# Optimization experiments

Measured on AMD Instinct MI355X. Metric: run time of the kernel, lower is better.

The kernel has to match this reference:

```python
import jax, jax.numpy as jnp
import numpy as np

HIDDEN = 1024
N_HEAD = 16
D_HEAD = HIDDEN // N_HEAD


def setup_inputs() -> dict:
    key = jax.random.key(0)
    ks = jax.random.split(key, 12)
    B, S, H = 2, 2048, HIDDEN
    scale = 1.0 / np.sqrt(H)
    inp = {
        "q": jax.random.normal(ks[0], (B, S, H), jnp.float32),
        "k": jax.random.normal(ks[1], (B, S, H), jnp.float32),
        "v": jax.random.normal(ks[2], (B, S, H), jnp.float32),
        "mask": jnp.ones((B, 1, S, S), jnp.int32),
        "w_q": jax.random.normal(ks[3], (H, H), jnp.float32) * scale,
        "b_q": jnp.zeros((H,), jnp.float32),
        "w_k": jax.random.normal(ks[4], (H, H), jnp.float32) * scale,
        "b_k": jnp.zeros((H,), jnp.float32),
        "w_v": jax.random.normal(ks[5], (H, H), jnp.float32) * scale,
        "b_v": jnp.zeros((H,), jnp.float32),
        "w_o": jax.random.normal(ks[6], (H, H), jnp.float32) * scale,
        "b_o": jnp.zeros((H,), jnp.float32),
    }
    return inp


def reference(q, k, v, mask, w_q, b_q, w_k, b_k, w_v, b_v, w_o, b_o):
    B, Sq, H = q.shape
    Sk = k.shape[1]
    # projections (weights stored as [in, out])
    qh = (q @ w_q + b_q).reshape(B, Sq, N_HEAD, D_HEAD).transpose(0, 2, 1, 3)
    kh = (k @ w_k + b_k).reshape(B, Sk, N_HEAD, D_HEAD).transpose(0, 2, 1, 3)
    vh = (v @ w_v + b_v).reshape(B, Sk, N_HEAD, D_HEAD).transpose(0, 2, 1, 3)
    scores = jnp.einsum("bhqd,bhkd->bhqk", qh, kh) * (D_HEAD ** -0.5)
    scores = jnp.where(mask == 0, jnp.float32(-10000.0), scores)
    attn = jax.nn.softmax(scores, axis=-1)
    out = jnp.einsum("bhqk,bhkd->bhqd", attn, vh)
    out = out.transpose(0, 2, 1, 3).reshape(B, Sq, H)
    return out @ w_o + b_o
```

## Files before the change

kernel.cpp:

```cpp
#include <hip/hip_runtime.h>
#include <hip/hip_bf16.h>
#include <stdint.h>

#define S_LEN 2048
#define HID   1024
#define NHEAD 16
#define DHEAD 64
#define BATCH 2

#define QSCALE 0.18033688f
#define MASKNEG -14427.0f

typedef __bf16 bf16_t;
typedef __bf16 bf16x4 __attribute__((ext_vector_type(4)));
typedef __bf16 bf16x8 __attribute__((ext_vector_type(8)));
typedef float  f32x4  __attribute__((ext_vector_type(4)));


__device__ __forceinline__ void gl_lds16(const bf16_t* g, bf16_t* l) {
  __builtin_amdgcn_global_load_lds((const __attribute__((address_space(1))) void*)g,
                                   (__attribute__((address_space(3))) void*)l,
                                   16, 0, 0);
}

template<int TR, int TC, int NW = 4>
__device__ __forceinline__ void stage_tile(const bf16_t* __restrict__ g, int ldg,
                                           bf16_t* lds, int wave, int lane) {
  constexpr int CH = TC / 8;
  constexpr int NINST = (TR * CH) / 64;
  #pragma unroll
  for (int i = wave; i < NINST; i += NW) {
    int slot = i * 64 + lane;
    int r  = slot / CH;
    int cs = slot & (CH - 1);
    int c  = cs ^ (r & (CH - 1));
    gl_lds16(g + (size_t)r * ldg + c * 8, lds + i * 512);
  }
}

template<int CH>
__device__ __forceinline__ bf16x8 frag_ld(const bf16_t* lds, int row, int kchunk) {
  int cs = kchunk ^ (row & (CH - 1));
  return *(const bf16x8*)(lds + (row * CH + cs) * 8);
}

__global__ __launch_bounds__(256) void preamble(
    const float* __restrict__ q, const float* __restrict__ k, const float* __restrict__ v,
    bf16_t* __restrict__ qb, bf16_t* __restrict__ kb, bf16_t* __restrict__ vb,
    const float* __restrict__ w0, const float* __restrict__ w1,
    const float* __restrict__ w2, const float* __restrict__ w3,
    bf16_t* __restrict__ wt, const int* __restrict__ mask, int* __restrict__ flags) {
  __shared__ float t[64][65];
  __shared__ int oks[16];
  int id = blockIdx.x;
  if (id < 12288) {
    int which = id >> 12;
    const float* src = which == 0 ? q : which == 1 ? k : v;
    bf16_t* dst = which == 0 ? qb : which == 1 ? kb : vb;
    size_t i = (((size_t)(id & 4095)) * 256 + threadIdx.x) * 4;
    float4 u = *(const float4*)(src + i);
    bf16x4 o = {(bf16_t)u.x, (bf16_t)u.y, (bf16_t)u.z, (bf16_t)u.w};
    *(bf16x4*)(dst + i) = o;
  } else if (id < 13312) {
    int tt = id - 12288;
    int bx = tt & 15, by = (tt >> 4) & 15, bz = tt >> 8;
    const float* W = bz == 0 ? w0 : bz == 1 ? w1 : bz == 2 ? w2 : w3;
    bf16_t* WT = wt + (size_t)bz * HID * HID;
    int tx = threadIdx.x & 63, ty = threadIdx.x >> 6;
    int r0 = by * 64, c0 = bx * 64;
    #pragma unroll
    for (int i = ty; i < 64; i += 4) t[i][tx] = W[(size_t)(r0 + i) * HID + c0 + tx];
    __syncthreads();
    #pragma unroll
    for (int i = ty; i < 64; i += 4) WT[(size_t)(c0 + i) * HID + r0 + tx] = (bf16_t)t[tx][i];
  } else {
    int tt = id - 13312;
    int qtile = tt & 15, rg = (tt >> 4) & 7, b = tt >> 7;
    const int* base = mask + (size_t)b * S_LEN * S_LEN
                    + (size_t)(qtile * 128 + rg * 16) * S_LEN;
    int tid = threadIdx.x;
    int kt = tid >> 4;
    int ok = 1;
    #pragma unroll
    for (int r = 0; r < 16; ++r) {
      const int4* p = (const int4*)(base + (size_t)r * S_LEN + tid * 8);
      int4 a = p[0], c = p[1];
      ok &= (a.x != 0) & (a.y != 0) & (a.z != 0) & (a.w != 0) &
            (c.x != 0) & (c.y != 0) & (c.z != 0) & (c.w != 0);
    }
    if (tid < 16) oks[tid] = -1;
    __syncthreads();
    if (!ok) atomicAnd(&oks[kt], 0);
    __syncthreads();
    if (tid < 16 && oks[tid] == 0) atomicAnd(&flags[(b * 16 + qtile) * 16 + tid], 0);
  }
}

__global__ __launch_bounds__(512) void qkv_gemm(
    const bf16_t* __restrict__ qb, const bf16_t* __restrict__ kb, const bf16_t* __restrict__ vb,
    const bf16_t* __restrict__ wT,
    const float* __restrict__ bq, const float* __restrict__ bk, const float* __restrict__ bv,
    bf16_t* __restrict__ Qh, bf16_t* __restrict__ Kh, bf16_t* __restrict__ VhT) {
  int mode = blockIdx.z;
  const bf16_t* A    = mode == 0 ? qb : mode == 1 ? kb : vb;
  const bf16_t* Bt   = wT + (size_t)mode * HID * HID;
  const float*  bias = mode == 0 ? bq : mode == 1 ? bk : bv;

  __shared__ __align__(16) bf16_t As[128 * 64];
  __shared__ __align__(16) bf16_t Bs[128 * 64];

  int tid = threadIdx.x, wave = tid >> 6, lane = tid & 63;
  int lane15 = lane & 15, quad = lane >> 4;
  int m0 = blockIdx.x * 128, n0 = blockIdx.y * 128;
  int wm = (wave & 3) * 32, wn = (wave >> 2) * 64;

  f32x4 zero4 = {0.f, 0.f, 0.f, 0.f};
  f32x4 acc[2][4];
  #pragma unroll
  for (int t = 0; t < 2; ++t)
    #pragma unroll
    for (int n = 0; n < 4; ++n) acc[t][n] = zero4;

  for (int k0 = 0; k0 < HID; k0 += 64) {
    stage_tile<128, 64, 8>(A  + (size_t)m0 * HID + k0, HID, As, wave, lane);
    stage_tile<128, 64, 8>(Bt + (size_t)n0 * HID + k0, HID, Bs, wave, lane);
    __syncthreads();
    #pragma unroll
    for (int kc = 0; kc < 2; ++kc) {
      bf16x8 af[2], bfr[4];
      #pragma unroll
      for (int t = 0; t < 2; ++t) af[t]  = frag_ld<8>(As, wm + t * 16 + lane15, kc * 4 + quad);
      #pragma unroll
      for (int n = 0; n < 4; ++n) bfr[n] = frag_ld<8>(Bs, wn + n * 16 + lane15, kc * 4 + quad);
      if (mode < 2) {
        #pragma unroll
        for (int t = 0; t < 2; ++t)
          #pragma unroll
          for (int n = 0; n < 4; ++n)
            acc[t][n] = __builtin_amdgcn_mfma_f32_16x16x32_bf16(af[t], bfr[n], acc[t][n], 0, 0, 0);
      } else {
        #pragma unroll
        for (int t = 0; t < 2; ++t)
          #pragma unroll
          for (int n = 0; n < 4; ++n)
            acc[t][n] = __builtin_amdgcn_mfma_f32_16x16x32_bf16(bfr[n], af[t], acc[t][n], 0, 0, 0);
      }
    }
    __syncthreads();
  }

  if (mode < 2) {
    float sc = (mode == 0) ? QSCALE : 1.0f;
    bf16_t* dst = (mode == 0 ? Qh : Kh);
    #pragma unroll
    for (int t = 0; t < 2; ++t) {
      #pragma unroll
      for (int n = 0; n < 4; ++n) {
        int col = n0 + wn + n * 16 + lane15;
        float bb = bias[col];
        #pragma unroll
        for (int i = 0; i < 4; ++i) {
          int row = m0 + wm + t * 16 + quad * 4 + i;
          bf16_t o = (bf16_t)((acc[t][n][i] + bb) * sc);
          int b = row >> 11, s = row & 2047;
          int h = col >> 6,  d = col & 63;
          dst[((size_t)(b * NHEAD + h) * S_LEN + s) * DHEAD + d] = o;
        }
      }
    }
  } else {
    #pragma unroll
    for (int n = 0; n < 4; ++n) {
      int dbase = n0 + wn + n * 16 + quad * 4;
      float4 bb4 = *(const float4*)(bias + dbase);
      #pragma unroll
      for (int t = 0; t < 2; ++t) {
        int token = m0 + wm + t * 16 + lane15;
        int b = token >> 11, s = token & 2047;
        #pragma unroll
        for (int i = 0; i < 4; ++i) {
          int dg = dbase + i;
          int h = dg >> 6, d = dg & 63;
          float bb = i == 0 ? bb4.x : i == 1 ? bb4.y : i == 2 ? bb4.z : bb4.w;
          VhT[((size_t)(b * NHEAD + h) * DHEAD + d) * S_LEN + s] = (bf16_t)(acc[t][n][i] + bb);
        }
      }
    }
  }
}

__global__ __launch_bounds__(512) void attn_kernel(
    const bf16_t* __restrict__ Qh, const bf16_t* __restrict__ Kh, const bf16_t* __restrict__ VhT,
    const int* __restrict__ mask, const int* __restrict__ flags,
    bf16_t* __restrict__ O) {
  __shared__ __align__(16) bf16_t Ks[4][64 * 64];
  __shared__ __align__(16) bf16_t VTs[4][64 * 64];
  __shared__ __align__(16) bf16_t Ps[128 * 64];

  int tid = threadIdx.x, wave = tid >> 6, lane = tid & 63;
  int lane15 = lane & 15, quad = lane >> 4;
  int L = blockIdx.x + (blockIdx.y << 4);
  int xcd = L & 7, slot = L >> 3;
  int bh = xcd + ((slot >> 4) << 3);
  int qt = slot & 15;
  int b = bh >> 4, h = bh & 15;
  int wrow = wave << 4;

  const bf16_t* Kbase = Kh + (size_t)bh * S_LEN * DHEAD;
  const bf16_t* Vbase = VhT + (size_t)bh * DHEAD * S_LEN;
  const int* flagrow = flags + (b * 16 + qt) * 16;

  int fmask = 0;
  #pragma unroll
  for (int j = 0; j < 16; ++j) fmask |= (flagrow[j] == 0 ? 1 : 0) << j;

  stage_tile<128, 64, 8>(Qh + ((size_t)bh * S_LEN + qt * 128) * DHEAD, DHEAD, Ps, wave, lane);
  stage_tile<64, 64, 8>(Kbase, DHEAD, Ks[0], wave, lane);
  stage_tile<64, 64, 8>(Vbase, S_LEN, VTs[0], wave, lane);
  stage_tile<64, 64, 8>(Kbase + (size_t)64 * DHEAD, DHEAD, Ks[1], wave, lane);
  stage_tile<64, 64, 8>(Vbase + 64, S_LEN, VTs[1], wave, lane);
  asm volatile("s_waitcnt vmcnt(4)" ::: "memory");
  __builtin_amdgcn_s_barrier();

  bf16x8 qa[2];
  #pragma unroll
  for (int kc = 0; kc < 2; ++kc)
    qa[kc] = frag_ld<8>(Ps, wrow + lane15, kc * 4 + quad);

  bf16x8 ones8;
  #pragma unroll
  for (int j = 0; j < 8; ++j) ones8[j] = (bf16_t)1.0f;

  f32x4 zero4 = {0.f, 0.f, 0.f, 0.f};
  f32x4 o_acc[5];
  #pragma unroll
  for (int mt = 0; mt < 5; ++mt) o_acc[mt] = zero4;

  for (int kt = 0; kt < S_LEN / 64; ++kt) {
    int nt = kt + 2 <= 31 ? kt + 2 : 31;
    int nbuf = (kt + 2) & 3;
    stage_tile<64, 64, 8>(Kbase + (size_t)nt * 64 * DHEAD, DHEAD, Ks[nbuf], wave, lane);
    stage_tile<64, 64, 8>(Vbase + nt * 64, S_LEN, VTs[nbuf], wave, lane);
    asm volatile("s_waitcnt vmcnt(4)" ::: "memory");
    __builtin_amdgcn_s_barrier();

    const bf16_t* Kc = Ks[kt & 3];
    const bf16_t* Vc = VTs[kt & 3];

    f32x4 sa[4];
    {
      bf16x8 kf[4];
      #pragma unroll
      for (int mc = 0; mc < 4; ++mc) kf[mc] = frag_ld<8>(Kc, mc * 16 + lane15, quad);
      __builtin_amdgcn_s_setprio(1);
      #pragma unroll
      for (int mc = 0; mc < 4; ++mc)
        sa[mc] = __builtin_amdgcn_mfma_f32_16x16x32_bf16(kf[mc], qa[0], zero4, 0, 0, 0);
      __builtin_amdgcn_s_setprio(0);
      #pragma unroll
      for (int mc = 0; mc < 4; ++mc) kf[mc] = frag_ld<8>(Kc, mc * 16 + lane15, 4 + quad);
      __builtin_amdgcn_s_setprio(1);
      #pragma unroll
      for (int mc = 0; mc < 4; ++mc)
        sa[mc] = __builtin_amdgcn_mfma_f32_16x16x32_bf16(kf[mc], qa[1], sa[mc], 0, 0, 0);
      __builtin_amdgcn_s_setprio(0);
    }

    if ((fmask >> (kt >> 1)) & 1) {
      int q = qt * 128 + wrow + lane15;
      #pragma unroll
      for (int mc = 0; mc < 4; ++mc)
        #pragma unroll
        for (int i = 0; i < 4; ++i) {
          int c = kt * 64 + mc * 16 + quad * 4 + i;
          if (mask[(size_t)b * S_LEN * S_LEN + (size_t)q * S_LEN + c] == 0)
            sa[mc][i] = MASKNEG;
        }
    }

    {
      int q = wrow + lane15;
      #pragma unroll
      for (int mc = 0; mc < 4; ++mc) {
        bf16x4 pk = {(bf16_t)exp2f(sa[mc][0]), (bf16_t)exp2f(sa[mc][1]),
                     (bf16_t)exp2f(sa[mc][2]), (bf16_t)exp2f(sa[mc][3])};
        int chunk = mc * 2 + (quad >> 1);
        int slot = chunk ^ (q & 7);
        *(bf16x4*)(Ps + q * 64 + slot * 8 + (quad & 1) * 4) = pk;
      }
    }

    #pragma unroll
    for (int kc = 0; kc < 2; ++kc) {
      bf16x8 vf[4], pf;
      #pragma unroll
      for (int mt = 0; mt < 4; ++mt) vf[mt] = frag_ld<8>(Vc, mt * 16 + lane15, kc * 4 + quad);
      pf = frag_ld<8>(Ps, wrow + lane15, kc * 4 + quad);
      __builtin_amdgcn_s_setprio(1);
      #pragma unroll
      for (int mt = 0; mt < 4; ++mt)
        o_acc[mt] = __builtin_amdgcn_mfma_f32_16x16x32_bf16(vf[mt], pf, o_acc[mt], 0, 0, 0);
      o_acc[4] = __builtin_amdgcn_mfma_f32_16x16x32_bf16(ones8, pf, o_acc[4], 0, 0, 0);
      __builtin_amdgcn_s_setprio(0);
    }
  }

  {
    float lval = __shfl(o_acc[4][0], lane15);
    float inv = 1.0f / lval;
    int s = qt * 128 + wrow + lane15;
    size_t orow = ((size_t)b * S_LEN + s) * HID + h * DHEAD;
    #pragma unroll
    for (int mt = 0; mt < 4; ++mt) {
      bf16x4 ov = {(bf16_t)(o_acc[mt][0] * inv), (bf16_t)(o_acc[mt][1] * inv),
                   (bf16_t)(o_acc[mt][2] * inv), (bf16_t)(o_acc[mt][3] * inv)};
      *(bf16x4*)(O + orow + mt * 16 + quad * 4) = ov;
    }
  }
}

__global__ __launch_bounds__(512) void oproj_gemm(
    const bf16_t* __restrict__ A, const bf16_t* __restrict__ Bt,
    const float* __restrict__ bias, float* __restrict__ out) {
  __shared__ __align__(16) bf16_t As[64 * 64];
  __shared__ __align__(16) bf16_t Bs[128 * 64];

  int tid = threadIdx.x, wave = tid >> 6, lane = tid & 63;
  int lane15 = lane & 15, quad = lane >> 4;
  int m0 = blockIdx.x * 64, n0 = blockIdx.y * 128;
  int wm = (wave & 1) * 32, wn = (wave >> 1) * 32;

  f32x4 zero4 = {0.f, 0.f, 0.f, 0.f};
  f32x4 acc[2][2];
  #pragma unroll
  for (int t = 0; t < 2; ++t)
    #pragma unroll
    for (int n = 0; n < 2; ++n) acc[t][n] = zero4;

  for (int k0 = 0; k0 < HID; k0 += 64) {
    stage_tile<64, 64, 8>(A  + (size_t)m0 * HID + k0, HID, As, wave, lane);
    stage_tile<128, 64, 8>(Bt + (size_t)n0 * HID + k0, HID, Bs, wave, lane);
    __syncthreads();
    #pragma unroll
    for (int kc = 0; kc < 2; ++kc) {
      bf16x8 af[2], bfr[2];
      #pragma unroll
      for (int t = 0; t < 2; ++t) af[t]  = frag_ld<8>(As, wm + t * 16 + lane15, kc * 4 + quad);
      #pragma unroll
      for (int n = 0; n < 2; ++n) bfr[n] = frag_ld<8>(Bs, wn + n * 16 + lane15, kc * 4 + quad);
      #pragma unroll
      for (int t = 0; t < 2; ++t)
        #pragma unroll
        for (int n = 0; n < 2; ++n)
          acc[t][n] = __builtin_amdgcn_mfma_f32_16x16x32_bf16(af[t], bfr[n], acc[t][n], 0, 0, 0);
    }
    __syncthreads();
  }

  #pragma unroll
  for (int t = 0; t < 2; ++t) {
    #pragma unroll
    for (int n = 0; n < 2; ++n) {
      int col = n0 + wn + n * 16 + lane15;
      float bb = bias[col];
      #pragma unroll
      for (int i = 0; i < 4; ++i) {
        int row = m0 + wm + t * 16 + quad * 4 + i;
        out[(size_t)row * HID + col] = acc[t][n][i] + bb;
      }
    }
  }
}

extern "C" void kernel_launch(void* const* d_in, const int* in_sizes, int n_in,
                              void* d_out, int out_size, void* d_ws, size_t ws_size,
                              hipStream_t stream) {
  (void)in_sizes; (void)n_in; (void)out_size; (void)ws_size;
  const float* q  = (const float*)d_in[0];
  const float* k  = (const float*)d_in[1];
  const float* v  = (const float*)d_in[2];
  const int*  mask = (const int*)d_in[3];
  const float* wq = (const float*)d_in[4];
  const float* bq = (const float*)d_in[5];
  const float* wk = (const float*)d_in[6];
  const float* bk = (const float*)d_in[7];
  const float* wv = (const float*)d_in[8];
  const float* bv = (const float*)d_in[9];
  const float* wo = (const float*)d_in[10];
  const float* bo = (const float*)d_in[11];

  char* ws = (char*)d_ws;
  bf16_t* wT    = (bf16_t*)(ws);
  bf16_t* Qh    = (bf16_t*)(ws + (8u  << 20));
  bf16_t* Kh    = (bf16_t*)(ws + (16u << 20));
  bf16_t* VhT   = (bf16_t*)(ws + (24u << 20));
  bf16_t* qb    = (bf16_t*)(ws + (32u << 20));
  bf16_t* kb    = (bf16_t*)(ws + (40u << 20));
  bf16_t* vb    = (bf16_t*)(ws + (48u << 20));
  int* flags    = (int*)(ws + (56u << 20));
  bf16_t* Obuf  = qb;

  hipMemsetAsync(flags, 0xFF, 512 * sizeof(int), stream);
  preamble<<<dim3(13568), 256, 0, stream>>>(q, k, v, qb, kb, vb,
                                            wq, wk, wv, wo, wT, mask, flags);
  qkv_gemm<<<dim3(32, 8, 3), 512, 0, stream>>>(qb, kb, vb, wT, bq, bk, bv, Qh, Kh, VhT);
  attn_kernel<<<dim3(16, 32), 512, 0, stream>>>(Qh, Kh, VhT, mask, flags, Obuf);
  oproj_gemm<<<dim3(64, 8), 512, 0, stream>>>(Obuf, wT + (size_t)3 * HID * HID, bo, (float*)d_out);
}
```

Measured before the change: 268.3 us.

## Double-buffer GEMM tile loads and replace mask-flag atomics with direct writes

The QKV and output-projection GEMMs now keep two LDS buffers for the A and B tiles. The next k-tile's global-to-LDS loads are issued before computing the current one, with explicit vmcnt waits and barriers, so memory latency overlaps MFMA work. The mask-flag preamble now has each row group write its own flag slot directly instead of doing atomicAnd into a shared slot. The attention kernel reduces the 8 row-group flags, which lets the memset launch be removed. In exchange the GEMMs use double the LDS, which may lower occupancy, and correctness depends on the vmcnt counts matching the number of loads stage_tile issues.

```diff
diff --git a/kernel.cpp b/kernel.cpp
--- a/kernel.cpp
+++ b/kernel.cpp
@@ -92,7 +92,7 @@
     __syncthreads();
     if (!ok) atomicAnd(&oks[kt], 0);
     __syncthreads();
-    if (tid < 16 && oks[tid] == 0) atomicAnd(&flags[(b * 16 + qtile) * 16 + tid], 0);
+    if (tid < 16) flags[(((b * 16) + qtile) * 8 + rg) * 16 + tid] = oks[tid];
   }
 }
 
@@ -106,14 +106,17 @@
   const bf16_t* Bt   = wT + (size_t)mode * HID * HID;
   const float*  bias = mode == 0 ? bq : mode == 1 ? bk : bv;
 
-  __shared__ __align__(16) bf16_t As[128 * 64];
-  __shared__ __align__(16) bf16_t Bs[128 * 64];
+  __shared__ __align__(16) bf16_t As[2][128 * 64];
+  __shared__ __align__(16) bf16_t Bs[2][128 * 64];
 
   int tid = threadIdx.x, wave = tid >> 6, lane = tid & 63;
   int lane15 = lane & 15, quad = lane >> 4;
   int m0 = blockIdx.x * 128, n0 = blockIdx.y * 128;
   int wm = (wave & 3) * 32, wn = (wave >> 2) * 64;
 
+  const bf16_t* Ab = A  + (size_t)m0 * HID;
+  const bf16_t* Bb = Bt + (size_t)n0 * HID;
+
   f32x4 zero4 = {0.f, 0.f, 0.f, 0.f};
   f32x4 acc[2][4];
   #pragma unroll
@@ -121,32 +124,42 @@
     #pragma unroll
     for (int n = 0; n < 4; ++n) acc[t][n] = zero4;
 
-  for (int k0 = 0; k0 < HID; k0 += 64) {
-    stage_tile<128, 64, 8>(A  + (size_t)m0 * HID + k0, HID, As, wave, lane);
-    stage_tile<128, 64, 8>(Bt + (size_t)n0 * HID + k0, HID, Bs, wave, lane);
-    __syncthreads();
+  stage_tile<128, 64, 8>(Ab, HID, As[0], wave, lane);
+  stage_tile<128, 64, 8>(Bb, HID, Bs[0], wave, lane);
+
+  for (int t = 0; t < 16; ++t) {
+    int cur = t & 1;
+    if (t < 15) {
+      stage_tile<128, 64, 8>(Ab + (t + 1) * 64, HID, As[cur ^ 1], wave, lane);
+      stage_tile<128, 64, 8>(Bb + (t + 1) * 64, HID, Bs[cur ^ 1], wave, lane);
+      asm volatile("s_waitcnt vmcnt(4)" ::: "memory");
+    } else {
+      asm volatile("s_waitcnt vmcnt(0)" ::: "memory");
+    }
+    __builtin_amdgcn_s_barrier();
+
     #pragma unroll
     for (int kc = 0; kc < 2; ++kc) {
       bf16x8 af[2], bfr[4];
       #pragma unroll
-      for (int t = 0; t < 2; ++t) af[t]  = frag_ld<8>(As, wm + t * 16 + lane15, kc * 4 + quad);
-      #pragma unroll
-      for (int n = 0; n < 4; ++n) bfr[n] = frag_ld<8>(Bs, wn + n * 16 + lane15, kc * 4 + quad);
+      for (int tt = 0; tt < 2; ++tt) af[tt] = frag_ld<8>(As[cur], wm + tt * 16 + lane15, kc * 4 + quad);
+      #pragma unroll
+      for (int n = 0; n < 4; ++n) bfr[n] = frag_ld<8>(Bs[cur], wn + n * 16 + lane15, kc * 4 + quad);
       if (mode < 2) {
         #pragma unroll
-        for (int t = 0; t < 2; ++t)
+        for (int tt = 0; tt < 2; ++tt)
           #pragma unroll
           for (int n = 0; n < 4; ++n)
-            acc[t][n] = __builtin_amdgcn_mfma_f32_16x16x32_bf16(af[t], bfr[n], acc[t][n], 0, 0, 0);
+            acc[tt][n] = __builtin_amdgcn_mfma_f32_16x16x32_bf16(af[tt], bfr[n], acc[tt][n], 0, 0, 0);
       } else {
         #pragma unroll
-        for (int t = 0; t < 2; ++t)
+        for (int tt = 0; tt < 2; ++tt)
           #pragma unroll
           for (int n = 0; n < 4; ++n)
-            acc[t][n] = __builtin_amdgcn_mfma_f32_16x16x32_bf16(bfr[n], af[t], acc[t][n], 0, 0, 0);
+            acc[tt][n] = __builtin_amdgcn_mfma_f32_16x16x32_bf16(bfr[n], af[tt], acc[tt][n], 0, 0, 0);
       }
     }
-    __syncthreads();
+    __builtin_amdgcn_s_barrier();
   }
 
   if (mode < 2) {
@@ -208,11 +221,14 @@
 
   const bf16_t* Kbase = Kh + (size_t)bh * S_LEN * DHEAD;
   const bf16_t* Vbase = VhT + (size_t)bh * DHEAD * S_LEN;
-  const int* flagrow = flags + (b * 16 + qt) * 16;
-
+
+  const int* f2 = flags + ((b * 16 + qt) * 8) * 16;
   int fmask = 0;
   #pragma unroll
-  for (int j = 0; j < 16; ++j) fmask |= (flagrow[j] == 0 ? 1 : 0) << j;
+  for (int rg = 0; rg < 8; ++rg)
+    #pragma unroll
+    for (int j = 0; j < 16; ++j)
+      fmask |= (f2[rg * 16 + j] == 0 ? 1 : 0) << j;
 
   stage_tile<128, 64, 8>(Qh + ((size_t)bh * S_LEN + qt * 128) * DHEAD, DHEAD, Ps, wave, lane);
   stage_tile<64, 64, 8>(Kbase, DHEAD, Ks[0], wave, lane);
@@ -322,14 +338,17 @@
 __global__ __launch_bounds__(512) void oproj_gemm(
     const bf16_t* __restrict__ A, const bf16_t* __restrict__ Bt,
     const float* __restrict__ bias, float* __restrict__ out) {
-  __shared__ __align__(16) bf16_t As[64 * 64];
-  __shared__ __align__(16) bf16_t Bs[128 * 64];
+  __shared__ __align__(16) bf16_t As[2][64 * 64];
+  __shared__ __align__(16) bf16_t Bs[2][128 * 64];
 
   int tid = threadIdx.x, wave = tid >> 6, lane = tid & 63;
   int lane15 = lane & 15, quad = lane >> 4;
   int m0 = blockIdx.x * 64, n0 = blockIdx.y * 128;
   int wm = (wave & 1) * 32, wn = (wave >> 1) * 32;
 
+  const bf16_t* Ab = A  + (size_t)m0 * HID;
+  const bf16_t* Bb = Bt + (size_t)n0 * HID;
+
   f32x4 zero4 = {0.f, 0.f, 0.f, 0.f};
   f32x4 acc[2][2];
   #pragma unroll
@@ -337,24 +356,34 @@
     #pragma unroll
     for (int n = 0; n < 2; ++n) acc[t][n] = zero4;
 
-  for (int k0 = 0; k0 < HID; k0 += 64) {
-    stage_tile<64, 64, 8>(A  + (size_t)m0 * HID + k0, HID, As, wave, lane);
-    stage_tile<128, 64, 8>(Bt + (size_t)n0 * HID + k0, HID, Bs, wave, lane);
-    __syncthreads();
+  stage_tile<64, 64, 8>(Ab, HID, As[0], wave, lane);
+  stage_tile<128, 64, 8>(Bb, HID, Bs[0], wave, lane);
+
+  for (int t = 0; t < 16; ++t) {
+    int cur = t & 1;
+    if (t < 15) {
+      stage_tile<64, 64, 8>(Ab + (t + 1) * 64, HID, As[cur ^ 1], wave, lane);
+      stage_tile<128, 64, 8>(Bb + (t + 1) * 64, HID, Bs[cur ^ 1], wave, lane);
+      asm volatile("s_waitcnt vmcnt(3)" ::: "memory");
+    } else {
+      asm volatile("s_waitcnt vmcnt(0)" ::: "memory");
+    }
+    __builtin_amdgcn_s_barrier();
+
     #pragma unroll
     for (int kc = 0; kc < 2; ++kc) {
       bf16x8 af[2], bfr[2];
       #pragma unroll
-      for (int t = 0; t < 2; ++t) af[t]  = frag_ld<8>(As, wm + t * 16 + lane15, kc * 4 + quad);
-      #pragma unroll
-      for (int n = 0; n < 2; ++n) bfr[n] = frag_ld<8>(Bs, wn + n * 16 + lane15, kc * 4 + quad);
-      #pragma unroll
-      for (int t = 0; t < 2; ++t)
+      for (int tt = 0; tt < 2; ++tt) af[tt] = frag_ld<8>(As[cur], wm + tt * 16 + lane15, kc * 4 + quad);
+      #pragma unroll
+      for (int n = 0; n < 2; ++n) bfr[n] = frag_ld<8>(Bs[cur], wn + n * 16 + lane15, kc * 4 + quad);
+      #pragma unroll
+      for (int tt = 0; tt < 2; ++tt)
         #pragma unroll
         for (int n = 0; n < 2; ++n)
-          acc[t][n] = __builtin_amdgcn_mfma_f32_16x16x32_bf16(af[t], bfr[n], acc[t][n], 0, 0, 0);
-    }
-    __syncthreads();
+          acc[tt][n] = __builtin_amdgcn_mfma_f32_16x16x32_bf16(af[tt], bfr[n], acc[tt][n], 0, 0, 0);
+    }
+    __builtin_amdgcn_s_barrier();
   }
 
   #pragma unroll
@@ -400,7 +429,6 @@
   int* flags    = (int*)(ws + (56u << 20));
   bf16_t* Obuf  = qb;
 
-  hipMemsetAsync(flags, 0xFF, 512 * sizeof(int), stream);
   preamble<<<dim3(13568), 256, 0, stream>>>(q, k, v, qb, kb, vb,
                                             wq, wk, wv, wo, wT, mask, flags);
   qkv_gemm<<<dim3(32, 8, 3), 512, 0, stream>>>(qb, kb, vb, wT, bq, bk, bv, Qh, Kh, VhT);
```

Measured after the change: 271.3 us. No clear change (+1.1%).
